# Performance work log

Measured on AMD Instinct MI355X. Metric: run time of the kernel, lower is better.

Reference implementation:

```python
import jax, jax.numpy as jnp
import numpy as np
import math

DIM_MODEL = 1024
N_HEAD = 16
NUM_NEURON = 64
MAX_LEN = 2048
B, S = 4, 2048


def setup_inputs() -> dict:
    key = jax.random.key(0)
    ks = jax.random.split(key, 11)
    d, p = DIM_MODEL, N_HEAD * NUM_NEURON
    sc_in = 1.0 / math.sqrt(d)
    sc_p = 1.0 / math.sqrt(p)
    return {
        "q": jax.random.normal(ks[0], (B, S, d), jnp.float32),
        "k": jax.random.normal(ks[1], (B, S, d), jnp.float32),
        "v": jax.random.normal(ks[2], (B, S, d), jnp.float32),
        "Wq": jax.random.normal(ks[3], (d, p), jnp.float32) * sc_in,
        "bq": jnp.zeros((p,), jnp.float32),
        "Wk": jax.random.normal(ks[4], (d, p), jnp.float32) * sc_in,
        "bk": jnp.zeros((p,), jnp.float32),
        "Wv": jax.random.normal(ks[5], (d, p), jnp.float32) * sc_in,
        "bv": jnp.zeros((p,), jnp.float32),
        "Wf": jax.random.normal(ks[6], (p, d), jnp.float32) * sc_p,
        "bf": jnp.zeros((d,), jnp.float32),
    }


def _split_heads(x):  # [B,S,H*Dh] -> [B,H,S,Dh]
    b, s, _ = x.shape
    return x.reshape(b, s, N_HEAD, NUM_NEURON).transpose(0, 2, 1, 3)


def reference(q, k, v, Wq, bq, Wk, bk, Wv, bv, Wf, bf):
    qh = _split_heads(q @ Wq + bq)
    kh = _split_heads(k @ Wk + bk)
    vh = _split_heads(v @ Wv + bv)
    # NOTE: original scales by 1/sqrt(max_len), not 1/sqrt(head_dim)
    scores = jnp.einsum("bhqd,bhkd->bhqk", qh, kh) / math.sqrt(MAX_LEN)
    s = scores.shape[-1]
    causal = jnp.tril(jnp.ones((s, s), bool))  # [S,S]
    scores = jnp.where(causal[None, None], scores, -jnp.inf)
    attn = jax.nn.softmax(scores, axis=-1)
    out = jnp.einsum("bhqk,bhkd->bhqd", attn, vh)  # [B,H,S,Dh]
    c = out.transpose(0, 2, 1, 3).reshape(out.shape[0], out.shape[2], N_HEAD * NUM_NEURON)
    return c @ Wf + bf
```

## Files before the change

### kernel.cpp

```cpp
#include <hip/hip_runtime.h>
#include <stdint.h>

#define DMODEL 1024
#define NHEAD 16
#define DH 64
#define BB 4
#define SS 2048
#define MROWS (BB * SS)

typedef __bf16 bfx8 __attribute__((ext_vector_type(8)));
typedef float f32x4 __attribute__((ext_vector_type(4)));
typedef float fvec4 __attribute__((ext_vector_type(4)));
typedef int i32x4 __attribute__((ext_vector_type(4)));
typedef unsigned short u16x8 __attribute__((ext_vector_type(8)));
typedef unsigned short u16x4 __attribute__((ext_vector_type(4)));

__device__ __forceinline__ unsigned short f2bf(float f) {
    union { float f; unsigned int u; } v; v.f = f;
    unsigned int r = v.u + 0x7FFFu + ((v.u >> 16) & 1u);
    return (unsigned short)(r >> 16);
}

__device__ __forceinline__ unsigned int cvtpk(float lo, float hi) {
    unsigned int r;
    asm("v_cvt_pk_bf16_f32 %0, %1, %2" : "=v"(r) : "v"(lo), "v"(hi));
    return r;
}

typedef __attribute__((address_space(1))) const void gas_t;
typedef __attribute__((address_space(3))) void las_t;
__device__ __forceinline__ void gload_lds16(const void* g, void* l) {
    __builtin_amdgcn_global_load_lds((gas_t*)g, (las_t*)l, 16, 0, 0);
}

__device__ __forceinline__ int sigma_k(int i) {
    return (i & 0x20) | ((i & 0x0C) << 1) | ((i & 0x10) >> 2) | (i & 3);
}

__global__ void cvt3_kernel(const float* __restrict__ s0, const float* __restrict__ s1,
                            const float* __restrict__ s2,
                            unsigned short* __restrict__ d0, unsigned short* __restrict__ d1,
                            unsigned short* __restrict__ d2, int n8)
{
    const float* s = (blockIdx.y == 0) ? s0 : (blockIdx.y == 1) ? s1 : s2;
    unsigned short* d = (blockIdx.y == 0) ? d0 : (blockIdx.y == 1) ? d1 : d2;
    int i = blockIdx.x * blockDim.x + threadIdx.x;
    if (i >= n8) return;
    fvec4 a = *reinterpret_cast<const fvec4*>(&s[(size_t)i * 8]);
    fvec4 b = *reinterpret_cast<const fvec4*>(&s[(size_t)i * 8 + 4]);
    u16x8 o;
    #pragma unroll
    for (int j = 0; j < 4; ++j) { o[j] = f2bf(a[j]); o[j + 4] = f2bf(b[j]); }
    *reinterpret_cast<u16x8*>(&d[(size_t)i * 8]) = o;
}

__global__ void transpose_cvt3_kernel(const float* __restrict__ W0, unsigned short* __restrict__ T0,
                                      const float* __restrict__ W1, unsigned short* __restrict__ T1,
                                      const float* __restrict__ W2, unsigned short* __restrict__ T2)
{
    const float* W = (blockIdx.z == 0) ? W0 : (blockIdx.z == 1) ? W1 : W2;
    unsigned short* Wt = (blockIdx.z == 0) ? T0 : (blockIdx.z == 1) ? T1 : T2;
    __shared__ unsigned short t[64][72];
    const int tid = threadIdx.x;
    const int r0 = blockIdx.y * 64, c0 = blockIdx.x * 64;
    #pragma unroll
    for (int i = 0; i < 4; ++i) {
        int idx = tid + i * 256;
        int r = idx >> 4, c4 = idx & 15;
        fvec4 v = *reinterpret_cast<const fvec4*>(&W[(size_t)(r0 + r) * DMODEL + c0 + c4 * 4]);
        #pragma unroll
        for (int j = 0; j < 4; ++j) t[c4 * 4 + j][r] = f2bf(v[j]);
    }
    __syncthreads();
    #pragma unroll
    for (int i = 0; i < 2; ++i) {
        int idx = tid + i * 256;
        int r = idx >> 3, c8 = idx & 7;
        u16x8 v = *reinterpret_cast<const u16x8*>(&t[r][c8 * 8]);
        *reinterpret_cast<u16x8*>(&Wt[(size_t)(c0 + r) * DMODEL + r0 + c8 * 8]) = v;
    }
}

struct GArg {
    const unsigned short* A;
    const unsigned short* Bt;
    const float* bias;
    void* O;
    float osc;
    int mode;
};

__global__ __launch_bounds__(256, 2)
void gemm_kernel(GArg g0, GArg g1, int M, int N, int K)
{
    const GArg g = blockIdx.z ? g1 : g0;
    __shared__ unsigned short sA[128 * 64];
    __shared__ unsigned short sB[128 * 64];
    const int tid  = threadIdx.x;
    const int lane = tid & 63;
    const int wave = tid >> 6;
    const int wm = (wave >> 1) * 64, wn = (wave & 1) * 64;
    const int m0 = blockIdx.x * 128, n0 = blockIdx.y * 128;
    const int lr = lane & 15;
    const int lg = lane >> 4;

    f32x4 acc[4][4] = {};

    for (int kk0 = 0; kk0 < K; kk0 += 64) {
        __syncthreads();
        #pragma unroll
        for (int i = 0; i < 4; ++i) {
            int c = tid + i * 256;
            int row = c >> 3, col8 = c & 7;
            gload_lds16(&g.A[(size_t)(m0 + row) * K + kk0 + col8 * 8], &sA[c * 8]);
        }
        #pragma unroll
        for (int i = 0; i < 4; ++i) {
            int c = tid + i * 256;
            int row = c >> 3, col8 = c & 7;
            gload_lds16(&g.Bt[(size_t)(n0 + row) * K + kk0 + col8 * 8], &sB[c * 8]);
        }
        __syncthreads();

        bfx8 af[4][2], bfr[4][2];
        #pragma unroll
        for (int m = 0; m < 4; ++m)
            #pragma unroll
            for (int kk = 0; kk < 2; ++kk)
                af[m][kk] = *reinterpret_cast<const bfx8*>(
                    &sA[(wm + m * 16 + lr) * 64 + kk * 32 + lg * 8]);
        #pragma unroll
        for (int n = 0; n < 4; ++n)
            #pragma unroll
            for (int kk = 0; kk < 2; ++kk)
                bfr[n][kk] = *reinterpret_cast<const bfx8*>(
                    &sB[(wn + n * 16 + lr) * 64 + kk * 32 + lg * 8]);
        #pragma unroll
        for (int kk = 0; kk < 2; ++kk)
            #pragma unroll
            for (int m = 0; m < 4; ++m)
                #pragma unroll
                for (int n = 0; n < 4; ++n)
                    acc[m][n] = __builtin_amdgcn_mfma_f32_16x16x32_bf16(
                        af[m][kk], bfr[n][kk], acc[m][n], 0, 0, 0);
    }

    #pragma unroll
    for (int n = 0; n < 4; ++n) {
        int col = n0 + wn + n * 16 + lr;
        float bv = g.bias[col];
        #pragma unroll
        for (int m = 0; m < 4; ++m) {
            int rowb = m0 + wm + m * 16 + lg * 4;
            float val[4];
            #pragma unroll
            for (int r = 0; r < 4; ++r) val[r] = (acc[m][n][r] + bv) * g.osc;
            if (g.mode == 0) {
                #pragma unroll
                for (int r = 0; r < 4; ++r)
                    ((unsigned short*)g.O)[(size_t)(rowb + r) * N + col] = f2bf(val[r]);
            } else if (g.mode == 2) {
                #pragma unroll
                for (int r = 0; r < 4; ++r)
                    ((float*)g.O)[(size_t)(rowb + r) * N + col] = val[r];
            } else {
                int bq = rowb >> 11, s = rowb & 2047;
                int hh = col >> 6, d = col & 63;
                u16x4 pk;
                #pragma unroll
                for (int r = 0; r < 4; ++r) pk[r] = f2bf(val[r]);
                size_t idx = ((size_t)(bq * 16 + hh) * 64 + d) * 2048 + s;
                *reinterpret_cast<u16x4*>(&((unsigned short*)g.O)[idx]) = pk;
            }
        }
    }
}

__global__ __launch_bounds__(512, 4)
void attn_kernel(const unsigned short* __restrict__ Q,
                 const unsigned short* __restrict__ K,
                 const unsigned short* __restrict__ Vt,
                 unsigned short* __restrict__ C)
{
    __shared__ unsigned short sK[4096];
    __shared__ unsigned short sV[4096];

    const int tid  = threadIdx.x;
    const int lane = tid & 63;
    const int wave = tid >> 6;
    const int lr = lane & 15, lg = lane >> 4;
    const int bh = blockIdx.x;
    const int p  = blockIdx.y;
    const int b = bh >> 4, h = bh & 15;
    const size_t rowbase = (size_t)b * SS;
    const int hcol = h * DH;

    const int srow = tid >> 3, sc8 = tid & 7;
    const int sig  = sigma_k(srow);
    const int woff = srow * 64 + ((sc8 ^ (srow & 7)) * 8);
    const int p0 = lg ^ (lr & 7);

    #pragma unroll
    for (int ph = 0; ph < 2; ++ph) {
        const int qt = ph ? p : (15 - p);
        const int q0 = qt * 128;

        bfx8 aq[2];
        {
            int qr = q0 + wave * 16 + lr;
            const unsigned short* qp = &Q[(rowbase + qr) * DMODEL + hcol + lg * 8];
            aq[0] = *reinterpret_cast<const bfx8*>(qp);
            aq[1] = *reinterpret_cast<const bfx8*>(qp + 32);
        }

        float m_run = 0.f;
        f32x4 l4 = {};
        f32x4 acc_o[4] = {};
        bool mz = true;
        const int qmax_wave = q0 + wave * 16 + 15;
        const int ntiles = 2 * qt + 2;

        u16x8 rk = *reinterpret_cast<const u16x8*>(
            &K[(rowbase + sig) * DMODEL + hcol + sc8 * 8]);
        u16x8 rv = *reinterpret_cast<const u16x8*>(
            &Vt[((size_t)bh * DH + srow) * SS + sc8 * 8]);

        for (int t = 0; t < ntiles; ++t) {
            __syncthreads();
            *reinterpret_cast<u16x8*>(&sK[woff]) = rk;
            *reinterpret_cast<u16x8*>(&sV[woff]) = rv;
            __syncthreads();
            if (t + 1 < ntiles) {
                const int kk = (t + 1) * 64;
                rk = *reinterpret_cast<const u16x8*>(
                    &K[(rowbase + kk + sig) * DMODEL + hcol + sc8 * 8]);
                rv = *reinterpret_cast<const u16x8*>(
                    &Vt[((size_t)bh * DH + srow) * SS + kk + sc8 * 8]);
            }
            const int k0 = t * 64;
            if (k0 > qmax_wave) continue;

            f32x4 sc[4];
            __builtin_amdgcn_s_setprio(1);
            #pragma unroll
            for (int nf = 0; nf < 4; ++nf) {
                int i = nf * 16 + lr;
                bfx8 ak0 = *reinterpret_cast<const bfx8*>(&sK[i * 64 + p0 * 8]);
                bfx8 ak1 = *reinterpret_cast<const bfx8*>(&sK[i * 64 + (p0 ^ 4) * 8]);
                f32x4 s = {0.f, 0.f, 0.f, 0.f};
                s = __builtin_amdgcn_mfma_f32_16x16x32_bf16(ak0, aq[0], s, 0, 0, 0);
                s = __builtin_amdgcn_mfma_f32_16x16x32_bf16(ak1, aq[1], s, 0, 0, 0);
                sc[nf] = s;
            }
            __builtin_amdgcn_s_setprio(0);
            if (k0 + 63 > q0 + wave * 16) {
                int qrow = q0 + wave * 16 + lr;
                #pragma unroll
                for (int nf = 0; nf < 4; ++nf) {
                    int kb = k0 + ((nf >> 1) << 5) + (lg << 3) + ((nf & 1) << 2);
                    #pragma unroll
                    for (int r = 0; r < 4; ++r)
                        if (kb + r > qrow) sc[nf][r] = -3.0e38f;
                }
            }
            f32x4 mx4 = sc[0];
            #pragma unroll
            for (int nf = 1; nf < 4; ++nf)
                #pragma unroll
                for (int r = 0; r < 4; ++r) mx4[r] = fmaxf(mx4[r], sc[nf][r]);
            float pmax = fmaxf(fmaxf(mx4[0], mx4[1]), fmaxf(mx4[2], mx4[3]));
            if (mz && __all(pmax <= 8.0f)) {
                #pragma unroll
                for (int nf = 0; nf < 4; ++nf) {
                    #pragma unroll
                    for (int r = 0; r < 4; ++r)
                        sc[nf][r] = __builtin_exp2f(sc[nf][r]);
                    l4 += sc[nf];
                }
            } else {
                mz = false;
                float mx = pmax;
                mx = fmaxf(mx, __shfl_xor(mx, 16, 64));
                mx = fmaxf(mx, __shfl_xor(mx, 32, 64));
                float mnew = fmaxf(m_run, mx);
                float fs = __builtin_exp2f(m_run - mnew);
                m_run = mnew;
                f32x4 ps = {0.f, 0.f, 0.f, 0.f};
                #pragma unroll
                for (int nf = 0; nf < 4; ++nf) {
                    #pragma unroll
                    for (int r = 0; r < 4; ++r)
                        sc[nf][r] = __builtin_exp2f(sc[nf][r] - mnew);
                    ps += sc[nf];
                }
                #pragma unroll
                for (int r = 0; r < 4; ++r) l4[r] = l4[r] * fs + ps[r];
                #pragma unroll
                for (int r = 0; r < 4; ++r) {
                    float fsa = __shfl(fs, lg * 4 + r, 64);
                    #pragma unroll
                    for (int d = 0; d < 4; ++d) acc_o[d][r] *= fsa;
                }
            }
            #pragma unroll
            for (int h2 = 0; h2 < 2; ++h2) {
                union { i32x4 i; bfx8 b; } pa;
                pa.i[0] = cvtpk(sc[2 * h2][0],     sc[2 * h2][1]);
                pa.i[1] = cvtpk(sc[2 * h2][2],     sc[2 * h2][3]);
                pa.i[2] = cvtpk(sc[2 * h2 + 1][0], sc[2 * h2 + 1][1]);
                pa.i[3] = cvtpk(sc[2 * h2 + 1][2], sc[2 * h2 + 1][3]);
                __builtin_amdgcn_s_setprio(1);
                #pragma unroll
                for (int d = 0; d < 4; ++d) {
                    int i = d * 16 + lr;
                    int pv = ((h2 << 2) | lg) ^ (lr & 7);
                    bfx8 bv0 = *reinterpret_cast<const bfx8*>(&sV[i * 64 + pv * 8]);
                    acc_o[d] = __builtin_amdgcn_mfma_f32_16x16x32_bf16(pa.b, bv0, acc_o[d], 0, 0, 0);
                }
                __builtin_amdgcn_s_setprio(0);
            }
        }

        float l = (l4[0] + l4[1]) + (l4[2] + l4[3]);
        l += __shfl_xor(l, 16, 64);
        l += __shfl_xor(l, 32, 64);
        float linv = 1.0f / l;
        float linva[4];
        #pragma unroll
        for (int r = 0; r < 4; ++r) linva[r] = __shfl(linv, lg * 4 + r, 64);
        const int qrb = q0 + wave * 16 + lg * 4;
        #pragma unroll
        for (int d = 0; d < 4; ++d) {
            int col = hcol + d * 16 + lr;
            #pragma unroll
            for (int r = 0; r < 4; ++r)
                C[(rowbase + qrb + r) * DMODEL + col] = f2bf(acc_o[d][r] * linva[r]);
        }
    }
}

extern "C" void kernel_launch(void* const* d_in, const int* in_sizes, int n_in,
                              void* d_out, int out_size, void* d_ws, size_t ws_size,
                              hipStream_t stream)
{
    const float* q  = (const float*)d_in[0];
    const float* k  = (const float*)d_in[1];
    const float* v  = (const float*)d_in[2];
    const float* Wq = (const float*)d_in[3];
    const float* bq = (const float*)d_in[4];
    const float* Wk = (const float*)d_in[5];
    const float* bk = (const float*)d_in[6];
    const float* Wv = (const float*)d_in[7];
    const float* bv = (const float*)d_in[8];
    const float* Wf = (const float*)d_in[9];
    const float* bf = (const float*)d_in[10];

    unsigned short* ws = (unsigned short*)d_ws;
    const size_t SZ = (size_t)MROWS * DMODEL;
    unsigned short* ws0 = ws;
    unsigned short* ws1 = ws + SZ;
    unsigned short* ws2 = ws + 2 * SZ;
    unsigned short* ws3 = ws + 3 * SZ;

    unsigned short* scr = (unsigned short*)d_out;
    unsigned short* WqT = scr;
    unsigned short* WkT = scr + 1048576;
    unsigned short* WvT = scr + 2097152;
    unsigned short* Qb  = scr + 4194304;

    const float qscale = 0.02209708691207961f * 1.44269504088896341f;

    const int n8 = (int)(SZ / 8);
    cvt3_kernel<<<dim3((n8 + 255) / 256, 3), 256, 0, stream>>>(q, k, v, ws0, ws1, ws2, n8);

    transpose_cvt3_kernel<<<dim3(16, 16, 3), 256, 0, stream>>>(Wq, WqT, Wk, WkT, Wv, WvT);

    {
        GArg gq{ws0, WqT, bq, Qb,  qscale, 0};
        GArg gk{ws1, WkT, bk, ws3, 1.0f,   0};
        gemm_kernel<<<dim3(64, 8, 2), 256, 0, stream>>>(gq, gk, MROWS, DMODEL, DMODEL);
    }
    {
        GArg gv{ws2, WvT, bv, ws0, 1.0f, 3};
        gemm_kernel<<<dim3(64, 8, 1), 256, 0, stream>>>(gv, gv, MROWS, DMODEL, DMODEL);
    }
    transpose_cvt3_kernel<<<dim3(16, 16, 1), 256, 0, stream>>>(Wf, ws2, Wf, ws2, Wf, ws2);

    attn_kernel<<<dim3(BB * NHEAD, 8), 512, 0, stream>>>(Qb, ws3, ws0, ws1);

    {
        GArg gf{ws1, ws2, bf, (float*)d_out, 1.0f, 2};
        gemm_kernel<<<dim3(64, 8, 1), 256, 0, stream>>>(gf, gf, MROWS, DMODEL, DMODEL);
    }
}
```

Measured before the change: 208.9 us.

## Process two KV tiles per barrier pair in attention; raise GEMM occupancy

The attention kernel now stages two 64-key K/V tiles into doubled LDS buffers per iteration. This halves the number of __syncthreads pairs and issues twice as many global prefetches ahead of compute. The GEMM kernel raises its launch-bounds occupancy hint from 2 to 4 blocks, and loads A/B fragments per k-substep instead of all at once to cut register pressure. Risks: more registers per thread for the doubled prefetch in attention, more LDS per block that may reduce attention occupancy, and possible GEMM spills under the tighter register budget.

```diff
diff --git a/kernel.cpp b/kernel.cpp
--- a/kernel.cpp
+++ b/kernel.cpp
@@ -90,7 +90,7 @@
     int mode;
 };
 
-__global__ __launch_bounds__(256, 2)
+__global__ __launch_bounds__(256, 4)
 void gemm_kernel(GArg g0, GArg g1, int M, int N, int K)
 {
     const GArg g = blockIdx.z ? g1 : g0;
@@ -122,27 +122,24 @@
         }
         __syncthreads();
 
-        bfx8 af[4][2], bfr[4][2];
-        #pragma unroll
-        for (int m = 0; m < 4; ++m)
-            #pragma unroll
-            for (int kk = 0; kk < 2; ++kk)
-                af[m][kk] = *reinterpret_cast<const bfx8*>(
+        #pragma unroll
+        for (int kk = 0; kk < 2; ++kk) {
+            bfx8 af[4], bfr[4];
+            #pragma unroll
+            for (int m = 0; m < 4; ++m)
+                af[m] = *reinterpret_cast<const bfx8*>(
                     &sA[(wm + m * 16 + lr) * 64 + kk * 32 + lg * 8]);
-        #pragma unroll
-        for (int n = 0; n < 4; ++n)
-            #pragma unroll
-            for (int kk = 0; kk < 2; ++kk)
-                bfr[n][kk] = *reinterpret_cast<const bfx8*>(
+            #pragma unroll
+            for (int n = 0; n < 4; ++n)
+                bfr[n] = *reinterpret_cast<const bfx8*>(
                     &sB[(wn + n * 16 + lr) * 64 + kk * 32 + lg * 8]);
-        #pragma unroll
-        for (int kk = 0; kk < 2; ++kk)
             #pragma unroll
             for (int m = 0; m < 4; ++m)
                 #pragma unroll
                 for (int n = 0; n < 4; ++n)
                     acc[m][n] = __builtin_amdgcn_mfma_f32_16x16x32_bf16(
-                        af[m][kk], bfr[n][kk], acc[m][n], 0, 0, 0);
+                        af[m], bfr[n], acc[m][n], 0, 0, 0);
+        }
     }
 
     #pragma unroll
@@ -182,8 +179,8 @@
                  const unsigned short* __restrict__ Vt,
                  unsigned short* __restrict__ C)
 {
-    __shared__ unsigned short sK[4096];
-    __shared__ unsigned short sV[4096];
+    __shared__ unsigned short sK[2 * 4096];
+    __shared__ unsigned short sV[2 * 4096];
 
     const int tid  = threadIdx.x;
     const int lane = tid & 63;
@@ -218,106 +215,119 @@
         f32x4 acc_o[4] = {};
         bool mz = true;
         const int qmax_wave = q0 + wave * 16 + 15;
-        const int ntiles = 2 * qt + 2;
-
-        u16x8 rk = *reinterpret_cast<const u16x8*>(
-            &K[(rowbase + sig) * DMODEL + hcol + sc8 * 8]);
-        u16x8 rv = *reinterpret_cast<const u16x8*>(
-            &Vt[((size_t)bh * DH + srow) * SS + sc8 * 8]);
-
-        for (int t = 0; t < ntiles; ++t) {
+        const int npairs = qt + 1;
+
+        u16x8 rk[2], rv[2];
+        #pragma unroll
+        for (int u = 0; u < 2; ++u) {
+            rk[u] = *reinterpret_cast<const u16x8*>(
+                &K[(rowbase + u * 64 + sig) * DMODEL + hcol + sc8 * 8]);
+            rv[u] = *reinterpret_cast<const u16x8*>(
+                &Vt[((size_t)bh * DH + srow) * SS + u * 64 + sc8 * 8]);
+        }
+
+        for (int u = 0; u < npairs; ++u) {
             __syncthreads();
-            *reinterpret_cast<u16x8*>(&sK[woff]) = rk;
-            *reinterpret_cast<u16x8*>(&sV[woff]) = rv;
+            #pragma unroll
+            for (int s = 0; s < 2; ++s) {
+                *reinterpret_cast<u16x8*>(&sK[s * 4096 + woff]) = rk[s];
+                *reinterpret_cast<u16x8*>(&sV[s * 4096 + woff]) = rv[s];
+            }
             __syncthreads();
-            if (t + 1 < ntiles) {
-                const int kk = (t + 1) * 64;
-                rk = *reinterpret_cast<const u16x8*>(
-                    &K[(rowbase + kk + sig) * DMODEL + hcol + sc8 * 8]);
-                rv = *reinterpret_cast<const u16x8*>(
-                    &Vt[((size_t)bh * DH + srow) * SS + kk + sc8 * 8]);
-            }
-            const int k0 = t * 64;
-            if (k0 > qmax_wave) continue;
-
-            f32x4 sc[4];
-            __builtin_amdgcn_s_setprio(1);
-            #pragma unroll
-            for (int nf = 0; nf < 4; ++nf) {
-                int i = nf * 16 + lr;
-                bfx8 ak0 = *reinterpret_cast<const bfx8*>(&sK[i * 64 + p0 * 8]);
-                bfx8 ak1 = *reinterpret_cast<const bfx8*>(&sK[i * 64 + (p0 ^ 4) * 8]);
-                f32x4 s = {0.f, 0.f, 0.f, 0.f};
-                s = __builtin_amdgcn_mfma_f32_16x16x32_bf16(ak0, aq[0], s, 0, 0, 0);
-                s = __builtin_amdgcn_mfma_f32_16x16x32_bf16(ak1, aq[1], s, 0, 0, 0);
-                sc[nf] = s;
-            }
-            __builtin_amdgcn_s_setprio(0);
-            if (k0 + 63 > q0 + wave * 16) {
-                int qrow = q0 + wave * 16 + lr;
-                #pragma unroll
-                for (int nf = 0; nf < 4; ++nf) {
-                    int kb = k0 + ((nf >> 1) << 5) + (lg << 3) + ((nf & 1) << 2);
-                    #pragma unroll
-                    for (int r = 0; r < 4; ++r)
-                        if (kb + r > qrow) sc[nf][r] = -3.0e38f;
+            if (u + 1 < npairs) {
+                #pragma unroll
+                for (int s = 0; s < 2; ++s) {
+                    const int kk = (2 * u + 2 + s) * 64;
+                    rk[s] = *reinterpret_cast<const u16x8*>(
+                        &K[(rowbase + kk + sig) * DMODEL + hcol + sc8 * 8]);
+                    rv[s] = *reinterpret_cast<const u16x8*>(
+                        &Vt[((size_t)bh * DH + srow) * SS + kk + sc8 * 8]);
                 }
             }
-            f32x4 mx4 = sc[0];
-            #pragma unroll
-            for (int nf = 1; nf < 4; ++nf)
-                #pragma unroll
-                for (int r = 0; r < 4; ++r) mx4[r] = fmaxf(mx4[r], sc[nf][r]);
-            float pmax = fmaxf(fmaxf(mx4[0], mx4[1]), fmaxf(mx4[2], mx4[3]));
-            if (mz && __all(pmax <= 8.0f)) {
+            #pragma unroll
+            for (int s = 0; s < 2; ++s) {
+                const int k0 = (2 * u + s) * 64;
+                if (k0 > qmax_wave) break;
+
+                f32x4 sc[4];
+                __builtin_amdgcn_s_setprio(1);
                 #pragma unroll
                 for (int nf = 0; nf < 4; ++nf) {
-                    #pragma unroll
-                    for (int r = 0; r < 4; ++r)
-                        sc[nf][r] = __builtin_exp2f(sc[nf][r]);
-                    l4 += sc[nf];
-                }
-            } else {
-                mz = false;
-                float mx = pmax;
-                mx = fmaxf(mx, __shfl_xor(mx, 16, 64));
-                mx = fmaxf(mx, __shfl_xor(mx, 32, 64));
-                float mnew = fmaxf(m_run, mx);
-                float fs = __builtin_exp2f(m_run - mnew);
-                m_run = mnew;
-                f32x4 ps = {0.f, 0.f, 0.f, 0.f};
-                #pragma unroll
-                for (int nf = 0; nf < 4; ++nf) {
-                    #pragma unroll
-                    for (int r = 0; r < 4; ++r)
-                        sc[nf][r] = __builtin_exp2f(sc[nf][r] - mnew);
-                    ps += sc[nf];
-                }
-                #pragma unroll
-                for (int r = 0; r < 4; ++r) l4[r] = l4[r] * fs + ps[r];
-                #pragma unroll
-                for (int r = 0; r < 4; ++r) {
-                    float fsa = __shfl(fs, lg * 4 + r, 64);
-                    #pragma unroll
-                    for (int d = 0; d < 4; ++d) acc_o[d][r] *= fsa;
-                }
-            }
-            #pragma unroll
-            for (int h2 = 0; h2 < 2; ++h2) {
-                union { i32x4 i; bfx8 b; } pa;
-                pa.i[0] = cvtpk(sc[2 * h2][0],     sc[2 * h2][1]);
-                pa.i[1] = cvtpk(sc[2 * h2][2],     sc[2 * h2][3]);
-                pa.i[2] = cvtpk(sc[2 * h2 + 1][0], sc[2 * h2 + 1][1]);
-                pa.i[3] = cvtpk(sc[2 * h2 + 1][2], sc[2 * h2 + 1][3]);
-                __builtin_amdgcn_s_setprio(1);
-                #pragma unroll
-                for (int d = 0; d < 4; ++d) {
-                    int i = d * 16 + lr;
-                    int pv = ((h2 << 2) | lg) ^ (lr & 7);
-                    bfx8 bv0 = *reinterpret_cast<const bfx8*>(&sV[i * 64 + pv * 8]);
-                    acc_o[d] = __builtin_amdgcn_mfma_f32_16x16x32_bf16(pa.b, bv0, acc_o[d], 0, 0, 0);
+                    int i = nf * 16 + lr;
+                    bfx8 ak0 = *reinterpret_cast<const bfx8*>(&sK[s * 4096 + i * 64 + p0 * 8]);
+                    bfx8 ak1 = *reinterpret_cast<const bfx8*>(&sK[s * 4096 + i * 64 + (p0 ^ 4) * 8]);
+                    f32x4 sv = {0.f, 0.f, 0.f, 0.f};
+                    sv = __builtin_amdgcn_mfma_f32_16x16x32_bf16(ak0, aq[0], sv, 0, 0, 0);
+                    sv = __builtin_amdgcn_mfma_f32_16x16x32_bf16(ak1, aq[1], sv, 0, 0, 0);
+                    sc[nf] = sv;
                 }
                 __builtin_amdgcn_s_setprio(0);
+                if (k0 + 63 > q0 + wave * 16) {
+                    int qrow = q0 + wave * 16 + lr;
+                    #pragma unroll
+                    for (int nf = 0; nf < 4; ++nf) {
+                        int kb = k0 + ((nf >> 1) << 5) + (lg << 3) + ((nf & 1) << 2);
+                        #pragma unroll
+                        for (int r = 0; r < 4; ++r)
+                            if (kb + r > qrow) sc[nf][r] = -3.0e38f;
+                    }
+                }
+                f32x4 mx4 = sc[0];
+                #pragma unroll
+                for (int nf = 1; nf < 4; ++nf)
+                    #pragma unroll
+                    for (int r = 0; r < 4; ++r) mx4[r] = fmaxf(mx4[r], sc[nf][r]);
+                float pmax = fmaxf(fmaxf(mx4[0], mx4[1]), fmaxf(mx4[2], mx4[3]));
+                if (mz && __all(pmax <= 8.0f)) {
+                    #pragma unroll
+                    for (int nf = 0; nf < 4; ++nf) {
+                        #pragma unroll
+                        for (int r = 0; r < 4; ++r)
+                            sc[nf][r] = __builtin_exp2f(sc[nf][r]);
+                        l4 += sc[nf];
+                    }
+                } else {
+                    mz = false;
+                    float mx = pmax;
+                    mx = fmaxf(mx, __shfl_xor(mx, 16, 64));
+                    mx = fmaxf(mx, __shfl_xor(mx, 32, 64));
+                    float mnew = fmaxf(m_run, mx);
+                    float fs = __builtin_exp2f(m_run - mnew);
+                    m_run = mnew;
+                    f32x4 ps = {0.f, 0.f, 0.f, 0.f};
+                    #pragma unroll
+                    for (int nf = 0; nf < 4; ++nf) {
+                        #pragma unroll
+                        for (int r = 0; r < 4; ++r)
+                            sc[nf][r] = __builtin_exp2f(sc[nf][r] - mnew);
+                        ps += sc[nf];
+                    }
+                    #pragma unroll
+                    for (int r = 0; r < 4; ++r) l4[r] = l4[r] * fs + ps[r];
+                    #pragma unroll
+                    for (int r = 0; r < 4; ++r) {
+                        float fsa = __shfl(fs, lg * 4 + r, 64);
+                        #pragma unroll
+                        for (int d = 0; d < 4; ++d) acc_o[d][r] *= fsa;
+                    }
+                }
+                #pragma unroll
+                for (int h2 = 0; h2 < 2; ++h2) {
+                    union { i32x4 i; bfx8 b; } pa;
+                    pa.i[0] = cvtpk(sc[2 * h2][0],     sc[2 * h2][1]);
+                    pa.i[1] = cvtpk(sc[2 * h2][2],     sc[2 * h2][3]);
+                    pa.i[2] = cvtpk(sc[2 * h2 + 1][0], sc[2 * h2 + 1][1]);
+                    pa.i[3] = cvtpk(sc[2 * h2 + 1][2], sc[2 * h2 + 1][3]);
+                    __builtin_amdgcn_s_setprio(1);
+                    #pragma unroll
+                    for (int d = 0; d < 4; ++d) {
+                        int i = d * 16 + lr;
+                        int pv = ((h2 << 2) | lg) ^ (lr & 7);
+                        bfx8 bv0 = *reinterpret_cast<const bfx8*>(&sV[s * 4096 + i * 64 + pv * 8]);
+                        acc_o[d] = __builtin_amdgcn_mfma_f32_16x16x32_bf16(pa.b, bv0, acc_o[d], 0, 0, 0);
+                    }
+                    __builtin_amdgcn_s_setprio(0);
+                }
             }
         }
 
```

Measured after the change: 196.0 us. -6.2%, faster.
